# Optimization experiments

Hardware: AMD Instinct MI355X
Metric: run time of the kernel (lower is better)

## Reference

```python
import jax, jax.numpy as jnp
import numpy as np

OBS = jnp.array([0, 3, 6, 9, 12])
LO, HI = 0.001, 2.0

def gamma(x):
    return LO + (HI - LO) * jax.nn.sigmoid(x)

def full_chain_rhs(y, k):
    # y: (B,13) species, k: (B,19) rate constants
    A, B_, C, D, E, F, G, H, I, J, K_, L, M = [y[..., i] for i in range(13)]
    (kf1, kf2, kf3, kf4, kf5, kf6, kf7, kf8, kf9, kf10, kf11, kf12,
     kr1, kr3, kr5, kr7, kr9, kr11, kr12) = [k[..., i] for i in range(19)]
    dA = -kf1 * A + kr1 * B_
    dB = kf1 * A - kr1 * B_ - kf2 * B_
    dC = kf2 * B_ - kf3 * C + kr3 * D
    dD = kf3 * C - kr3 * D - kf4 * D
    dE = kf4 * D - kf5 * E + kr5 * F
    dF = kf5 * E - kr5 * F - kf6 * F
    dG = kf6 * F - kf7 * G + kr7 * H
    dH = kf7 * G - kr7 * H - kf8 * H
    dI = kf8 * H - kf9 * I + kr9 * J
    dJ = kf9 * I - kr9 * J - kf10 * J
    dK = kf10 * J - kf11 * K_ + kr11 * L
    dL = kf11 * K_ - kr11 * L - kf12 * L + kr12 * M
    dM = kf12 * L - kr12 * M
    return jnp.stack([dA, dB, dC, dD, dE, dF, dG, dH, dI, dJ, dK, dL, dM], axis=-1)

def rk4_step(y, dt, k):
    # y:(B,13) dt:(B,1) k:(B,19)
    k1 = full_chain_rhs(y, k)
    k2 = full_chain_rhs(y + 0.5 * dt * k1, k)
    k3 = full_chain_rhs(y + 0.5 * dt * k2, k)
    k4 = full_chain_rhs(y + dt * k3, k)
    return jnp.maximum(y + dt / 6.0 * (k1 + 2.0 * k2 + 2.0 * k3 + k4), 0.0)

def setup_inputs() -> dict:
    B, K, U, P = 2048, 256, 4, 5
    LIFT, HID = 32, 128
    key = jax.random.key(0)
    ks = jax.random.split(key, 9)
    in_dim = U + P
    def xavier(k, shape):
        lim = np.sqrt(6.0 / (shape[0] + shape[1])).astype(np.float32)
        return jax.random.uniform(k, shape, jnp.float32, -lim, lim)
    return {
        "y0": jax.random.uniform(ks[0], (B, P), jnp.float32),
        "u_seq": jax.random.normal(ks[1], (B, K, U), jnp.float32) * 0.1,
        "dt_seq": jax.random.uniform(ks[2], (B, K), jnp.float32, 0.01, 0.1),
        "y_seq": jax.random.uniform(ks[3], (B, K, P), jnp.float32),
        "W_lift": xavier(ks[4], (in_dim, LIFT)),
        "b_lift": jnp.zeros((LIFT,), jnp.float32),
        "w_ih": xavier(ks[5], (3 * HID, LIFT)),
        "w_hh": xavier(ks[6], (3 * HID, HID)),
        "b_ih": jnp.zeros((3 * HID,), jnp.float32),
        "b_hh": jnp.zeros((3 * HID,), jnp.float32),
        "W_head": xavier(ks[7], (HID, 19)),
        "b_head": jnp.zeros((19,), jnp.float32),
        "u_to_y_jump": jax.random.normal(ks[8], (U, P), jnp.float32) * 0.05,
        "tf_every": 50,
    }

def reference(y0, u_seq, dt_seq, y_seq, W_lift, b_lift, w_ih, w_hh, b_ih, b_hh, W_head, b_head, u_to_y_jump, tf_every):
    B, K, _ = u_seq.shape
    HID = w_hh.shape[1]
    # init hidden full state: 0.01 everywhere, obs slots get y0 + 0.01
    y_full0 = jnp.full((B, 13), 0.01, u_seq.dtype).at[:, OBS].set(y0 + 0.01)
    h0 = jnp.zeros((B, HID), u_seq.dtype)
    t = jnp.arange(K)
    tf_mask = (t > 0) & (t % tf_every == 0)  # teacher-forcing steps
    y_seq_prev = jnp.concatenate([jnp.zeros_like(y_seq[:, :1]), y_seq[:, :-1]], axis=1)
    xs = (jnp.swapaxes(u_seq, 0, 1), dt_seq.T[..., None],
          jnp.swapaxes(y_seq_prev, 0, 1), tf_mask)

    def step(carry, x):
        y_full, h = carry
        u_k, dt_k, y_prev_tf, m = x
        y_obs_prev = y_full[:, OBS]
        y_prev_in = jax.lax.stop_gradient(jnp.where(m, y_prev_tf, y_obs_prev))
        feat = jnp.concatenate([u_k, y_prev_in], axis=-1)
        lifted = jax.nn.silu(feat @ W_lift + b_lift)
        # PyTorch GRU cell
        gx = lifted @ w_ih.T + b_ih
        gh = h @ w_hh.T + b_hh
        rx, zx, nx = jnp.split(gx, 3, axis=-1)
        rh, zh, nh = jnp.split(gh, 3, axis=-1)
        r = jax.nn.sigmoid(rx + rh)
        z = jax.nn.sigmoid(zx + zh)
        n = jnp.tanh(nx + r * nh)
        h_new = (1.0 - z) * n + z * h
        theta = gamma(h_new @ W_head + b_head)  # (B,19), all bounds (0.001,2.0)
        y_obs_jump = y_obs_prev + u_k @ u_to_y_jump
        y_full_jump = y_full.at[:, OBS].set(y_obs_jump)
        y_full_next = rk4_step(y_full_jump, dt_k, theta)  # n_sub=1 as in forward
        return (y_full_next, h_new), (y_full_next[:, OBS], theta)

    _, (y_out, theta_out) = jax.lax.scan(step, (y_full0, h0), xs)
    return jnp.swapaxes(y_out, 0, 1), jnp.swapaxes(theta_out, 0, 1)
```

## Files before the change

### kernel.cpp

```cpp
#include <hip/hip_runtime.h>
#include <cstddef>
#include <cstdint>

#define NB 8
#define NTHREADS 640
#define HID 128
#define LIFT 32
#define NSP 13
#define NTH 19

typedef __attribute__((ext_vector_type(8))) short short8;
typedef __attribute__((ext_vector_type(4))) float f32x4;

__device__ const int   c_kA [13] = {0,0,1,2,3,4,5,6,7,8,9,10,11};
__device__ const int   c_kB1[13] = {0,12,2,13,4,14,6,15,8,16,10,17,18};
__device__ const int   c_kB2[13] = {0,1,0,3,0,5,0,7,0,9,0,11,0};
__device__ const int   c_kC [13] = {12,0,13,0,14,0,15,0,16,0,17,18,0};
__device__ const float c_mA [13] = {0.f,1.f,1.f,1.f,1.f,1.f,1.f,1.f,1.f,1.f,1.f,1.f,1.f};
__device__ const float c_mB2[13] = {0.f,1.f,0.f,1.f,0.f,1.f,0.f,1.f,0.f,1.f,0.f,1.f,0.f};
__device__ const float c_mC [13] = {1.f,0.f,1.f,0.f,1.f,0.f,1.f,0.f,1.f,0.f,1.f,1.f,0.f};

__device__ __forceinline__ uint32_t pk(float a, float b) {
  uint32_t ua = __float_as_uint(a), ub = __float_as_uint(b);
  ua = (ua + 0x7FFFu + ((ua >> 16) & 1u)) >> 16;
  ub = (ub + 0x7FFFu + ((ub >> 16) & 1u)) >> 16;
  return ua | (ub << 16);
}
__device__ __forceinline__ float sigm(float a) { return 1.f/(1.f + __expf(-a)); }

__device__ __forceinline__ void sync_lds() {
  __builtin_amdgcn_sched_barrier(0);
  asm volatile("s_waitcnt lgkmcnt(0)" ::: "memory");
  __builtin_amdgcn_s_barrier();
  __builtin_amdgcn_sched_barrier(0);
}

__device__ __forceinline__ float rhs3(int am1, int ap1, float cA, float cB,
                                      float cC, float yc) {
  const float ym1 = __int_as_float(__builtin_amdgcn_ds_bpermute(am1, __float_as_int(yc)));
  const float yp1 = __int_as_float(__builtin_amdgcn_ds_bpermute(ap1, __float_as_int(yc)));
  return fmaf(cA, ym1, fmaf(cB, yc, cC * yp1));
}

union FragU { uint4 u; short8 s; };
__device__ __forceinline__ short8 ldfrag(const float* p) {
  FragU t;
  const float4 a = *reinterpret_cast<const float4*>(p);
  const float4 b = *reinterpret_cast<const float4*>(p+4);
  t.u = make_uint4(pk(a.x,a.y), pk(a.z,a.w), pk(b.x,b.y), pk(b.z,b.w));
  return t.s;
}

struct Smem {
  uint32_t whdF[2*4*64*4];
  uint32_t hF[4*64*4];
  uint32_t liftF[64*4];
  float theta[8*20];
};

__global__ __launch_bounds__(NTHREADS, 3)
void fullmodel_rnn(const float* __restrict__ y0,
                   const float* __restrict__ u_seq,
                   const float* __restrict__ dt_seq,
                   const float* __restrict__ y_seq,
                   const float* __restrict__ W_lift,
                   const float* __restrict__ b_lift,
                   const float* __restrict__ w_ih,
                   const float* __restrict__ w_hh,
                   const float* __restrict__ b_ih,
                   const float* __restrict__ b_hh,
                   const float* __restrict__ W_head,
                   const float* __restrict__ b_head,
                   const float* __restrict__ u2y,
                   const int*  __restrict__ tf_every_p,
                   float* __restrict__ out,
                   int K, int theta_off)
{
  extern __shared__ __align__(16) char smem_raw[];
  Smem& S = *reinterpret_cast<Smem*>(smem_raw);

  const int tid  = threadIdx.x;
  const int wid  = tid >> 6;
  const int lane = tid & 63;
  const int q    = lane >> 4;
  const int col  = lane & 15;
  const int bg0  = blockIdx.x * NB;
  const int tf_every = tf_every_p[0];
  const bool gatew = (wid < 8);

  for (int f = tid; f < 2*4*64; f += NTHREADS) {
    int l = f & 63, idx = f >> 6;
    int s = idx & 3, T = idx >> 2;
    int o = 16*T + (l & 15);
    int k0 = 32*s + 8*(l >> 4);
    uint32_t* d = S.whdF + (size_t)f*4;
    if (o < NTH) {
#pragma unroll
      for (int c=0;c<4;++c)
        d[c] = pk(W_head[(size_t)(k0+2*c)*NTH + o], W_head[(size_t)(k0+2*c+1)*NTH + o]);
    } else {
#pragma unroll
      for (int c=0;c<4;++c) d[c] = 0u;
    }
  }
  for (int f = tid; f < 4*64*4; f += NTHREADS) S.hF[f] = 0u;
  for (int f = tid; f < 64*4;   f += NTHREADS) S.liftF[f] = 0u;

  const uint32_t* hf_p  = &S.hF[lane*4];
  const uint32_t* lf_p  = &S.liftF[lane*4];
  const uint32_t* whdp  = S.whdF + (size_t)lane*4;

  float bsumR[4], bsumZ[4], bihn_[4], bhhn_[4], h_old[4];
  short8 wfR[4], wfZ[4], wfN[4], wir, wiz, win;
  if (gatew) {
    const int rowR = 16*wid + col, kq = 8*q;
    wir = ldfrag(w_ih + (size_t)rowR*LIFT + kq);
    wiz = ldfrag(w_ih + (size_t)(128+rowR)*LIFT + kq);
    win = ldfrag(w_ih + (size_t)(256+rowR)*LIFT + kq);
    const float* wb = w_hh + (size_t)rowR*HID + kq;
#pragma unroll
    for (int ss=0; ss<4; ++ss) {
      wfR[ss] = ldfrag(wb + 32*ss);
      wfZ[ss] = ldfrag(wb + (size_t)128*HID + 32*ss);
      wfN[ss] = ldfrag(wb + (size_t)256*HID + 32*ss);
    }
#pragma unroll
    for (int r2=0;r2<4;++r2) {
      const int i0 = 16*wid + 4*q + r2;
      bsumR[r2] = b_ih[i0]     + b_hh[i0];
      bsumZ[r2] = b_ih[128+i0] + b_hh[128+i0];
      bihn_[r2] = b_ih[256+i0];
      bhhn_[r2] = b_hh[256+i0];
      h_old[r2] = 0.f;
    }
  }

  float bhd[2][4] = {{0,0,0,0},{0,0,0,0}};
  float wa0=0,wa1=0,wa2=0,wa3=0,wa4=0,wa5=0,wa6=0,wa7=0,wa8=0;
  float wb0=0,wb1=0,wb2=0,wb3=0,wb4=0,wb5=0,wb6=0,wb7=0,wb8=0;
  float blA=0.f, blB=0.f;
  const int base_b = (wid == 9) ? 4 : 0;
  const int b_loc = lane / NSP, rs = lane - NSP*b_loc;
  const bool rk_lane = (!gatew) && (lane < 52);
  const int bl8 = base_b + b_loc;
  const int gb = bg0 + (rk_lane ? bl8 : 0);
  const bool obs = rk_lane && (rs % 3 == 0);
  const int ro = rs / 3;
  float y_reg=0.f, u_cur=0.f, f_src=0.f;
  float u2yv[4]={0,0,0,0};
  int kA_=0,kB1_=0,kB2_=0,kC_=0;
  float mA_=0.f,mB2_=0.f,mC_=0.f;
  int am1=0, ap1=0, tfc=1;
  float dt_c=0.f, ysq_c=0.f, u_n=0.f;
  float* outT0 = out; float* outY = out;
  if (!gatew) {
#pragma unroll
    for (int T=0;T<2;++T)
#pragma unroll
      for (int r2=0;r2<4;++r2) {
        const int o = 16*T + 4*q + r2;
        bhd[T][r2] = (o < NTH) ? b_head[o] : 0.f;
      }
    const int li = 2*col;
    wa0=W_lift[0*32+li]; wa1=W_lift[1*32+li]; wa2=W_lift[2*32+li];
    wa3=W_lift[3*32+li]; wa4=W_lift[4*32+li]; wa5=W_lift[5*32+li];
    wa6=W_lift[6*32+li]; wa7=W_lift[7*32+li]; wa8=W_lift[8*32+li];
    wb0=W_lift[0*32+li+1]; wb1=W_lift[1*32+li+1]; wb2=W_lift[2*32+li+1];
    wb3=W_lift[3*32+li+1]; wb4=W_lift[4*32+li+1]; wb5=W_lift[5*32+li+1];
    wb6=W_lift[6*32+li+1]; wb7=W_lift[7*32+li+1]; wb8=W_lift[8*32+li+1];
    blA = b_lift[li]; blB = b_lift[li+1];
    outT0 = out + (size_t)theta_off + ((size_t)(bg0+col))*K*NTH + 4*q;
    __builtin_amdgcn_s_setprio(2);
  }
  if (rk_lane) {
    kA_ = c_kA[rs]; kB1_ = c_kB1[rs]; kB2_ = c_kB2[rs]; kC_ = c_kC[rs];
    mA_ = c_mA[rs]; mB2_ = c_mB2[rs]; mC_ = c_mC[rs];
    am1 = 4 * ((lane > 0)  ? (lane - 1) : 0);
    ap1 = 4 * ((lane < 51) ? (lane + 1) : 51);
    y_reg = 0.01f + (obs ? y0[gb*5 + ro] : 0.f);
    if (rs < 4) u_cur = u_seq[(size_t)gb*K*4 + rs];
    if (obs) { for (int d=0;d<4;++d) u2yv[d] = u2y[d*5 + ro]; }
    f_src = y_reg;
    outY = out + ((size_t)gb*K)*5 + ro;
  }
  sync_lds();

  for (int k = 0; k <= K; ++k) {
    f32x4 accR={0,0,0,0}, accZ={0,0,0,0}, accNH={0,0,0,0};

    if (gatew) {
      if (k < K) {
        FragU h0,h1,h2,h3;
        h0.u = *reinterpret_cast<const uint4*>(hf_p);
        h1.u = *reinterpret_cast<const uint4*>(hf_p + 256);
        h2.u = *reinterpret_cast<const uint4*>(hf_p + 512);
        h3.u = *reinterpret_cast<const uint4*>(hf_p + 768);
#pragma unroll
        for (int ss=0; ss<4; ++ss) {
          const short8 hb = (ss==0)?h0.s:(ss==1)?h1.s:(ss==2)?h2.s:h3.s;
          accR  = __builtin_amdgcn_mfma_f32_16x16x32_bf16(wfR[ss], hb, accR, 0,0,0);
          accZ  = __builtin_amdgcn_mfma_f32_16x16x32_bf16(wfZ[ss], hb, accZ, 0,0,0);
          accNH = __builtin_amdgcn_mfma_f32_16x16x32_bf16(wfN[ss], hb, accNH, 0,0,0);
        }
      }
    } else {
      float dt_p=0.f, ysq_p=0.f, u_p=0.f;
      if (rk_lane && k < K) {
        if (rs == 4)              dt_p  = dt_seq[(size_t)gb*K + k];
        if (obs)                  ysq_p = y_seq[((size_t)gb*K + k)*5 + ro];
        if (rs < 4 && (k+1) < K)  u_p   = u_seq[((size_t)gb*K + (k+1))*4 + rs];
      }
      if (k >= 1) {
        f32x4 at0={0,0,0,0}, at1={0,0,0,0};
        FragU h0,h1,h2,h3;
        h0.u = *reinterpret_cast<const uint4*>(hf_p);
        h1.u = *reinterpret_cast<const uint4*>(hf_p + 256);
        h2.u = *reinterpret_cast<const uint4*>(hf_p + 512);
        h3.u = *reinterpret_cast<const uint4*>(hf_p + 768);
#pragma unroll
        for (int ss=0; ss<4; ++ss) {
          FragU a0,a1;
          a0.u = *reinterpret_cast<const uint4*>(whdp + (0*4+ss)*256);
          a1.u = *reinterpret_cast<const uint4*>(whdp + (1*4+ss)*256);
          const short8 hb = (ss==0)?h0.s:(ss==1)?h1.s:(ss==2)?h2.s:h3.s;
          at0 = __builtin_amdgcn_mfma_f32_16x16x32_bf16(a0.s, hb, at0, 0,0,0);
          at1 = __builtin_amdgcn_mfma_f32_16x16x32_bf16(a1.s, hb, at1, 0,0,0);
        }
        if (col >= base_b && col < base_b + 4) {
          f32x4 th0;
#pragma unroll
          for (int r2=0;r2<4;++r2) th0[r2] = 0.001f + 1.999f*sigm(at0[r2] + bhd[0][r2]);
          *reinterpret_cast<f32x4*>(&S.theta[col*20 + 4*q]) = th0;
          outT0[0]=th0[0]; outT0[1]=th0[1]; outT0[2]=th0[2]; outT0[3]=th0[3];
          if (q == 0) {
            f32x4 th1;
#pragma unroll
            for (int r2=0;r2<4;++r2) th1[r2] = 0.001f + 1.999f*sigm(at1[r2] + bhd[1][r2]);
            *reinterpret_cast<f32x4*>(&S.theta[col*20 + 16]) = th1;
            outT0[16]=th1[0]; outT0[17]=th1[1]; outT0[18]=th1[2];
          }
        }
        if (rk_lane) {
          const float dtv = __shfl(dt_c, NSP*b_loc + 4);
          const float u0 = __shfl(u_cur, NSP*b_loc + 0);
          const float u1 = __shfl(u_cur, NSP*b_loc + 1);
          const float u2 = __shfl(u_cur, NSP*b_loc + 2);
          const float u3 = __shfl(u_cur, NSP*b_loc + 3);
          const float* thp = S.theta + bl8*20;
          const float cA = mA_ * thp[kA_];
          const float cB = -(thp[kB1_] + mB2_ * thp[kB2_]);
          const float cC = mC_ * thp[kC_];
          float yj = y_reg;
          if (obs) yj += u0*u2yv[0] + u1*u2yv[1] + u2*u2yv[2] + u3*u2yv[3];
          float yc = yj;
          const float k1 = rhs3(am1, ap1, cA, cB, cC, yc);
          yc = fmaf(0.5f*dtv, k1, yj);
          const float k2 = rhs3(am1, ap1, cA, cB, cC, yc);
          yc = fmaf(0.5f*dtv, k2, yj);
          const float k3 = rhs3(am1, ap1, cA, cB, cC, yc);
          yc = fmaf(dtv, k3, yj);
          const float k4 = rhs3(am1, ap1, cA, cB, cC, yc);
          const float yn = fmaxf(fmaf(dtv*(1.f/6.f), k1 + 2.f*k2 + 2.f*k3 + k4, yj), 0.f);
          y_reg = yn;
          if (obs) *outY = yn;
          if (k < K) {
            const bool m_next = (tfc == tf_every);
            tfc = m_next ? 1 : (tfc + 1);
            u_cur = u_n;
            if (obs) f_src = m_next ? ysq_c : yn;
          }
        }
        outT0 += NTH; outY += 5;
      }
      if (k < K) {
        const int g4 = NSP*(lane >> 4);
        const float fu0 = __shfl(u_cur, g4+0), fu1 = __shfl(u_cur, g4+1);
        const float fu2 = __shfl(u_cur, g4+2), fu3 = __shfl(u_cur, g4+3);
        const float fy0 = __shfl(f_src, g4+0), fy1 = __shfl(f_src, g4+3);
        const float fy2 = __shfl(f_src, g4+6), fy3 = __shfl(f_src, g4+9);
        const float fy4 = __shfl(f_src, g4+12);
        float a = blA + fu0*wa0 + fu1*wa1 + fu2*wa2 + fu3*wa3
                      + fy0*wa4 + fy1*wa5 + fy2*wa6 + fy3*wa7 + fy4*wa8;
        float b = blB + fu0*wb0 + fu1*wb1 + fu2*wb2 + fu3*wb3
                      + fy0*wb4 + fy1*wb5 + fy2*wb6 + fy3*wb7 + fy4*wb8;
        const float va = a*sigm(a), vb = b*sigm(b);
        const int bL = base_b + (lane >> 4);
        S.liftF[(col>>2)*64 + bL*4 + (col&3)] = pk(va, vb);
      }
      dt_c = dt_p; ysq_c = ysq_p; u_n = u_p;
    }
    sync_lds();

    if (gatew && k < K) {
      FragU lf; lf.u = *reinterpret_cast<const uint4*>(lf_p);
      accR = __builtin_amdgcn_mfma_f32_16x16x32_bf16(wir, lf.s, accR, 0,0,0);
      accZ = __builtin_amdgcn_mfma_f32_16x16x32_bf16(wiz, lf.s, accZ, 0,0,0);
      f32x4 z4 = {0,0,0,0};
      f32x4 accNX = __builtin_amdgcn_mfma_f32_16x16x32_bf16(win, lf.s, z4, 0,0,0);
      float hn[4];
#pragma unroll
      for (int r2=0;r2<4;++r2) {
        const float rg = sigm(accR[r2] + bsumR[r2]);
        const float zg = sigm(accZ[r2] + bsumZ[r2]);
        const float nx = accNX[r2] + bihn_[r2];
        const float nh = accNH[r2] + bhhn_[r2];
        const float e  = __expf(2.f*(nx + rg*nh));
        const float ng = 1.f - 2.f/(e + 1.f);
        hn[r2] = (1.f - zg)*ng + zg*h_old[r2];
        h_old[r2] = hn[r2];
      }
      const int word = (wid>>1)*256 + ((((2*wid)+(q>>1))&3)*16 + col)*4 + 2*(q&1);
      *reinterpret_cast<uint2*>(&S.hF[word]) = make_uint2(pk(hn[0],hn[1]), pk(hn[2],hn[3]));
    }
    sync_lds();
  }
}

extern "C" void kernel_launch(void* const* d_in, const int* in_sizes, int n_in,
                              void* d_out, int out_size, void* d_ws, size_t ws_size,
                              hipStream_t stream) {
  const float* y0     = (const float*)d_in[0];
  const float* u_seq  = (const float*)d_in[1];
  const float* dt_seq = (const float*)d_in[2];
  const float* y_seq  = (const float*)d_in[3];
  const float* W_lift = (const float*)d_in[4];
  const float* b_lift = (const float*)d_in[5];
  const float* w_ih   = (const float*)d_in[6];
  const float* w_hh   = (const float*)d_in[7];
  const float* b_ih   = (const float*)d_in[8];
  const float* b_hh   = (const float*)d_in[9];
  const float* W_head = (const float*)d_in[10];
  const float* b_head = (const float*)d_in[11];
  const float* u2y    = (const float*)d_in[12];
  const int*   tfe    = (const int*)d_in[13];
  float* out = (float*)d_out;

  const int B = in_sizes[0] / 5;
  const int K = in_sizes[2] / B;
  const int theta_off = B * K * 5;

  (void)hipFuncSetAttribute((const void*)fullmodel_rnn,
                            hipFuncAttributeMaxDynamicSharedMemorySize,
                            (int)sizeof(Smem));

  dim3 grid(B / NB), block(NTHREADS);
  hipLaunchKernelGGL(fullmodel_rnn, grid, block, sizeof(Smem), stream,
                     y0, u_seq, dt_seq, y_seq, W_lift, b_lift, w_ih, w_hh,
                     b_ih, b_hh, W_head, b_head, u2y, tfe, out, K, theta_off);
}
```

Before: 767.1 us.

## Move w_hh MFMA fragments from registers to LDS and simplify RK coefficient lookup

The recurrent weight fragments, which were held in 48 VGPRs per gate lane, now live in LDS and are reloaded every step before the MFMAs. The minimum-occupancy hint in launch bounds is dropped. Each RK lane now loads dt and the u vector directly as float4 rather than getting them through shuffles. The per-species mask multiplies are replaced by indexing a zeroed theta slot 19. The aim is lower register pressure and fewer shuffles, at the cost of extra LDS traffic on the serial critical path and a much larger shared memory footprint per block.

```diff
diff --git a/kernel.cpp b/kernel.cpp
--- a/kernel.cpp
+++ b/kernel.cpp
@@ -12,13 +12,10 @@
 typedef __attribute__((ext_vector_type(8))) short short8;
 typedef __attribute__((ext_vector_type(4))) float f32x4;
 
-__device__ const int   c_kA [13] = {0,0,1,2,3,4,5,6,7,8,9,10,11};
-__device__ const int   c_kB1[13] = {0,12,2,13,4,14,6,15,8,16,10,17,18};
-__device__ const int   c_kB2[13] = {0,1,0,3,0,5,0,7,0,9,0,11,0};
-__device__ const int   c_kC [13] = {12,0,13,0,14,0,15,0,16,0,17,18,0};
-__device__ const float c_mA [13] = {0.f,1.f,1.f,1.f,1.f,1.f,1.f,1.f,1.f,1.f,1.f,1.f,1.f};
-__device__ const float c_mB2[13] = {0.f,1.f,0.f,1.f,0.f,1.f,0.f,1.f,0.f,1.f,0.f,1.f,0.f};
-__device__ const float c_mC [13] = {1.f,0.f,1.f,0.f,1.f,0.f,1.f,0.f,1.f,0.f,1.f,1.f,0.f};
+__device__ const int c_kA [13] = {19,0,1,2,3,4,5,6,7,8,9,10,11};
+__device__ const int c_kB1[13] = {0,12,2,13,4,14,6,15,8,16,10,17,18};
+__device__ const int c_kB2[13] = {19,1,19,3,19,5,19,7,19,9,19,11,19};
+__device__ const int c_kC [13] = {12,19,13,19,14,19,15,19,16,19,17,18,19};
 
 __device__ __forceinline__ uint32_t pk(float a, float b) {
   uint32_t ua = __float_as_uint(a), ub = __float_as_uint(b);
@@ -52,13 +49,14 @@
 }
 
 struct Smem {
+  uint32_t whF[8*3*4*64*4];
   uint32_t whdF[2*4*64*4];
   uint32_t hF[4*64*4];
   uint32_t liftF[64*4];
   float theta[8*20];
 };
 
-__global__ __launch_bounds__(NTHREADS, 3)
+__global__ __launch_bounds__(NTHREADS)
 void fullmodel_rnn(const float* __restrict__ y0,
                    const float* __restrict__ u_seq,
                    const float* __restrict__ dt_seq,
@@ -88,6 +86,16 @@
   const int tf_every = tf_every_p[0];
   const bool gatew = (wid < 8);
 
+  for (int f = tid; f < 8*3*4*64; f += NTHREADS) {
+    int l = f & 63, idx = f >> 6;
+    int s = idx & 3; idx >>= 2;
+    int g = idx % 3, w = idx / 3;
+    int row = 128*g + 16*w + (l & 15);
+    int k0 = 32*s + 8*(l >> 4);
+    const float* p = w_hh + (size_t)row*HID + k0;
+    uint32_t* d = S.whF + (size_t)f*4;
+    d[0]=pk(p[0],p[1]); d[1]=pk(p[2],p[3]); d[2]=pk(p[4],p[5]); d[3]=pk(p[6],p[7]);
+  }
   for (int f = tid; f < 2*4*64; f += NTHREADS) {
     int l = f & 63, idx = f >> 6;
     int s = idx & 3, T = idx >> 2;
@@ -105,25 +113,20 @@
   }
   for (int f = tid; f < 4*64*4; f += NTHREADS) S.hF[f] = 0u;
   for (int f = tid; f < 64*4;   f += NTHREADS) S.liftF[f] = 0u;
+  if (tid < 8) S.theta[tid*20 + 19] = 0.f;
 
   const uint32_t* hf_p  = &S.hF[lane*4];
   const uint32_t* lf_p  = &S.liftF[lane*4];
+  const uint32_t* whp   = S.whF + ((size_t)wid*12*64 + lane)*4;
   const uint32_t* whdp  = S.whdF + (size_t)lane*4;
 
   float bsumR[4], bsumZ[4], bihn_[4], bhhn_[4], h_old[4];
-  short8 wfR[4], wfZ[4], wfN[4], wir, wiz, win;
+  short8 wir, wiz, win;
   if (gatew) {
     const int rowR = 16*wid + col, kq = 8*q;
     wir = ldfrag(w_ih + (size_t)rowR*LIFT + kq);
     wiz = ldfrag(w_ih + (size_t)(128+rowR)*LIFT + kq);
     win = ldfrag(w_ih + (size_t)(256+rowR)*LIFT + kq);
-    const float* wb = w_hh + (size_t)rowR*HID + kq;
-#pragma unroll
-    for (int ss=0; ss<4; ++ss) {
-      wfR[ss] = ldfrag(wb + 32*ss);
-      wfZ[ss] = ldfrag(wb + (size_t)128*HID + 32*ss);
-      wfN[ss] = ldfrag(wb + (size_t)256*HID + 32*ss);
-    }
 #pragma unroll
     for (int r2=0;r2<4;++r2) {
       const int i0 = 16*wid + 4*q + r2;
@@ -144,14 +147,15 @@
   const bool rk_lane = (!gatew) && (lane < 52);
   const int bl8 = base_b + b_loc;
   const int gb = bg0 + (rk_lane ? bl8 : 0);
+  const int gbL = bg0 + base_b + (lane >> 4);
   const bool obs = rk_lane && (rs % 3 == 0);
   const int ro = rs / 3;
-  float y_reg=0.f, u_cur=0.f, f_src=0.f;
+  float y_reg=0.f, f_src=0.f;
   float u2yv[4]={0,0,0,0};
   int kA_=0,kB1_=0,kB2_=0,kC_=0;
-  float mA_=0.f,mB2_=0.f,mC_=0.f;
   int am1=0, ap1=0, tfc=1;
-  float dt_c=0.f, ysq_c=0.f, u_n=0.f;
+  float dt_c=0.f, ysq_c=0.f;
+  float4 ujc = {0,0,0,0};
   float* outT0 = out; float* outY = out;
   if (!gatew) {
 #pragma unroll
@@ -174,11 +178,9 @@
   }
   if (rk_lane) {
     kA_ = c_kA[rs]; kB1_ = c_kB1[rs]; kB2_ = c_kB2[rs]; kC_ = c_kC[rs];
-    mA_ = c_mA[rs]; mB2_ = c_mB2[rs]; mC_ = c_mC[rs];
     am1 = 4 * ((lane > 0)  ? (lane - 1) : 0);
     ap1 = 4 * ((lane < 51) ? (lane + 1) : 51);
     y_reg = 0.01f + (obs ? y0[gb*5 + ro] : 0.f);
-    if (rs < 4) u_cur = u_seq[(size_t)gb*K*4 + rs];
     if (obs) { for (int d=0;d<4;++d) u2yv[d] = u2y[d*5 + ro]; }
     f_src = y_reg;
     outY = out + ((size_t)gb*K)*5 + ro;
@@ -197,18 +199,26 @@
         h3.u = *reinterpret_cast<const uint4*>(hf_p + 768);
 #pragma unroll
         for (int ss=0; ss<4; ++ss) {
+          FragU ar,az,an;
+          ar.u = *reinterpret_cast<const uint4*>(whp + (0*4+ss)*256);
+          az.u = *reinterpret_cast<const uint4*>(whp + (1*4+ss)*256);
+          an.u = *reinterpret_cast<const uint4*>(whp + (2*4+ss)*256);
           const short8 hb = (ss==0)?h0.s:(ss==1)?h1.s:(ss==2)?h2.s:h3.s;
-          accR  = __builtin_amdgcn_mfma_f32_16x16x32_bf16(wfR[ss], hb, accR, 0,0,0);
-          accZ  = __builtin_amdgcn_mfma_f32_16x16x32_bf16(wfZ[ss], hb, accZ, 0,0,0);
-          accNH = __builtin_amdgcn_mfma_f32_16x16x32_bf16(wfN[ss], hb, accNH, 0,0,0);
+          accR  = __builtin_amdgcn_mfma_f32_16x16x32_bf16(ar.s, hb, accR, 0,0,0);
+          accZ  = __builtin_amdgcn_mfma_f32_16x16x32_bf16(az.s, hb, accZ, 0,0,0);
+          accNH = __builtin_amdgcn_mfma_f32_16x16x32_bf16(an.s, hb, accNH, 0,0,0);
         }
       }
     } else {
-      float dt_p=0.f, ysq_p=0.f, u_p=0.f;
-      if (rk_lane && k < K) {
-        if (rs == 4)              dt_p  = dt_seq[(size_t)gb*K + k];
-        if (obs)                  ysq_p = y_seq[((size_t)gb*K + k)*5 + ro];
-        if (rs < 4 && (k+1) < K)  u_p   = u_seq[((size_t)gb*K + (k+1))*4 + rs];
+      float dt_p=0.f, ysq_p=0.f;
+      float4 ujp = {0,0,0,0}, ul = {0,0,0,0};
+      if (k < K) {
+        if (rk_lane) {
+          dt_p = dt_seq[(size_t)gb*K + k];
+          ujp  = *reinterpret_cast<const float4*>(u_seq + ((size_t)gb*K + k)*4);
+          if (obs) ysq_p = y_seq[((size_t)gb*K + k)*5 + ro];
+        }
+        ul = *reinterpret_cast<const float4*>(u_seq + ((size_t)gbL*K + k)*4);
       }
       if (k >= 1) {
         f32x4 at0={0,0,0,0}, at1={0,0,0,0};
@@ -236,22 +246,19 @@
             f32x4 th1;
 #pragma unroll
             for (int r2=0;r2<4;++r2) th1[r2] = 0.001f + 1.999f*sigm(at1[r2] + bhd[1][r2]);
+            outT0[16]=th1[0]; outT0[17]=th1[1]; outT0[18]=th1[2];
+            th1[3] = 0.f;
             *reinterpret_cast<f32x4*>(&S.theta[col*20 + 16]) = th1;
-            outT0[16]=th1[0]; outT0[17]=th1[1]; outT0[18]=th1[2];
           }
         }
         if (rk_lane) {
-          const float dtv = __shfl(dt_c, NSP*b_loc + 4);
-          const float u0 = __shfl(u_cur, NSP*b_loc + 0);
-          const float u1 = __shfl(u_cur, NSP*b_loc + 1);
-          const float u2 = __shfl(u_cur, NSP*b_loc + 2);
-          const float u3 = __shfl(u_cur, NSP*b_loc + 3);
+          const float dtv = dt_c;
           const float* thp = S.theta + bl8*20;
-          const float cA = mA_ * thp[kA_];
-          const float cB = -(thp[kB1_] + mB2_ * thp[kB2_]);
-          const float cC = mC_ * thp[kC_];
+          const float cA = thp[kA_];
+          const float cB = -(thp[kB1_] + thp[kB2_]);
+          const float cC = thp[kC_];
           float yj = y_reg;
-          if (obs) yj += u0*u2yv[0] + u1*u2yv[1] + u2*u2yv[2] + u3*u2yv[3];
+          if (obs) yj += ujc.x*u2yv[0] + ujc.y*u2yv[1] + ujc.z*u2yv[2] + ujc.w*u2yv[3];
           float yc = yj;
           const float k1 = rhs3(am1, ap1, cA, cB, cC, yc);
           yc = fmaf(0.5f*dtv, k1, yj);
@@ -266,7 +273,6 @@
           if (k < K) {
             const bool m_next = (tfc == tf_every);
             tfc = m_next ? 1 : (tfc + 1);
-            u_cur = u_n;
             if (obs) f_src = m_next ? ysq_c : yn;
           }
         }
@@ -274,20 +280,18 @@
       }
       if (k < K) {
         const int g4 = NSP*(lane >> 4);
-        const float fu0 = __shfl(u_cur, g4+0), fu1 = __shfl(u_cur, g4+1);
-        const float fu2 = __shfl(u_cur, g4+2), fu3 = __shfl(u_cur, g4+3);
         const float fy0 = __shfl(f_src, g4+0), fy1 = __shfl(f_src, g4+3);
         const float fy2 = __shfl(f_src, g4+6), fy3 = __shfl(f_src, g4+9);
         const float fy4 = __shfl(f_src, g4+12);
-        float a = blA + fu0*wa0 + fu1*wa1 + fu2*wa2 + fu3*wa3
+        float a = blA + ul.x*wa0 + ul.y*wa1 + ul.z*wa2 + ul.w*wa3
                       + fy0*wa4 + fy1*wa5 + fy2*wa6 + fy3*wa7 + fy4*wa8;
-        float b = blB + fu0*wb0 + fu1*wb1 + fu2*wb2 + fu3*wb3
+        float b = blB + ul.x*wb0 + ul.y*wb1 + ul.z*wb2 + ul.w*wb3
                       + fy0*wb4 + fy1*wb5 + fy2*wb6 + fy3*wb7 + fy4*wb8;
         const float va = a*sigm(a), vb = b*sigm(b);
         const int bL = base_b + (lane >> 4);
         S.liftF[(col>>2)*64 + bL*4 + (col&3)] = pk(va, vb);
       }
-      dt_c = dt_p; ysq_c = ysq_p; u_n = u_p;
+      dt_c = dt_p; ysq_c = ysq_p; ujc = ujp;
     }
     sync_lds();
 
```

After: 647.1 us, median of 2. -15.6%, faster.
